# Kernel tuning notes

Hardware: AMD Instinct MI355X
Metric: run time of the kernel (lower is better)

Reference implementation:

```python
import jax, jax.numpy as jnp
import numpy as np

B, T, C = 4, 2048, 1024
H = 16
DH = C // H  # 64


def setup_inputs() -> dict:
    key = jax.random.key(0)
    ks = jax.random.split(key, 10)
    s_in = 1.0 / np.sqrt(C)
    x = jax.random.normal(ks[0], (B, T, C), dtype=jnp.float32)
    # stacked per-head projection weights: [H, C, DH]
    Wq = jax.random.normal(ks[1], (H, C, DH), dtype=jnp.float32) * s_in
    bq = jnp.zeros((H, DH), dtype=jnp.float32)
    Wk = jax.random.normal(ks[2], (H, C, DH), dtype=jnp.float32) * s_in
    bk = jnp.zeros((H, DH), dtype=jnp.float32)
    Wv = jax.random.normal(ks[3], (H, C, DH), dtype=jnp.float32) * s_in
    bv = jnp.zeros((H, DH), dtype=jnp.float32)
    Wo = jax.random.normal(ks[4], (C, C), dtype=jnp.float32) * s_in
    bo = jnp.zeros((C,), dtype=jnp.float32)
    return {"x": x, "Wq": Wq, "bq": bq, "Wk": Wk, "bk": bk,
            "Wv": Wv, "bv": bv, "Wo": Wo, "bo": bo}


def reference(x, Wq, bq, Wk, bk, Wv, bv, Wo, bo):
    # per-head projections: (B,T,C) x (H,C,DH) -> (B,H,T,DH)
    q = jnp.einsum('btc,hcd->bhtd', x, Wq) + bq[None, :, None, :]
    k = jnp.einsum('btc,hcd->bhtd', x, Wk) + bk[None, :, None, :]
    v = jnp.einsum('btc,hcd->bhtd', x, Wv) + bv[None, :, None, :]
    # scores scaled by C**-0.5 (C = full input embedding dim, as in source)
    scale = jnp.float32(C) ** -0.5
    scores = jnp.einsum('bhtd,bhsd->bhts', q, k) * scale  # (B,H,T,T)
    causal = jnp.tril(jnp.ones((T, T), dtype=bool))
    scores = jnp.where(causal, scores, -jnp.inf)
    attn = jax.nn.softmax(scores, axis=-1)
    out = jnp.einsum('bhts,bhsd->bhtd', attn, v)  # (B,H,T,DH)
    out = out.transpose(0, 2, 1, 3).reshape(B, T, C)  # concat heads
    return out @ Wo + bo
```

## Files before the change

### kernel.cpp

```cpp
#include <hip/hip_runtime.h>
#include <hip/hip_bf16.h>

#define TDIM 2048
#define BDIM 4
#define CDIM 1024
#define HDIM 16
#define DH   64

typedef __hip_bfloat16 bf16;
typedef __attribute__((ext_vector_type(8))) short bf16x8;
typedef __attribute__((ext_vector_type(4))) short bf16x4;
typedef __attribute__((ext_vector_type(4))) float f32x4;

__device__ __forceinline__ void async_ld16(const bf16* g, bf16* l) {
    __builtin_amdgcn_global_load_lds(
        (const __attribute__((address_space(1))) unsigned int*)g,
        (__attribute__((address_space(3))) unsigned int*)l, 16, 0, 0);
}

__device__ __forceinline__ unsigned short bf16bits(float x) {
    bf16 b = __float2bfloat16(x);
    return *(unsigned short*)&b;
}

__device__ __forceinline__ f32x4 mfma_16x16x16_bf16(bf16x4 a, bf16x4 b, f32x4 c) {
#if __has_builtin(__builtin_amdgcn_mfma_f32_16x16x16_bf16)
    return __builtin_amdgcn_mfma_f32_16x16x16_bf16(a, b, c, 0, 0, 0);
#elif __has_builtin(__builtin_amdgcn_mfma_f32_16x16x16bf16_1k)
    return __builtin_amdgcn_mfma_f32_16x16x16bf16_1k(a, b, c, 0, 0, 0);
#else
    asm volatile("v_mfma_f32_16x16x16_bf16 %0, %1, %2, %0"
                 : "+v"(c) : "v"(a), "v"(b));
    return c;
#endif
}

__global__ void convert_x4(const float4* __restrict__ src, ushort4* __restrict__ dst, int n4) {
    int i = blockIdx.x * blockDim.x + threadIdx.x;
    if (i >= n4) return;
    float4 v = src[i];
    ushort4 o;
    o.x = bf16bits(v.x); o.y = bf16bits(v.y);
    o.z = bf16bits(v.z); o.w = bf16bits(v.w);
    dst[i] = o;
}

__global__ void convert_biases(const float* __restrict__ b0, const float* __restrict__ b1,
                               const float* __restrict__ b2, const float* __restrict__ b3,
                               bf16* __restrict__ dst) {
    int i = blockIdx.x * blockDim.x + threadIdx.x;
    int which = i >> 10, j = i & 1023;
    const float* src = (which == 0) ? b0 : (which == 1) ? b1 : (which == 2) ? b2 : b3;
    dst[i] = __float2bfloat16(src[j]);
}

__global__ __launch_bounds__(256) void transpose_qkv_kernel(
    const float* __restrict__ Wq, const float* __restrict__ Wk, const float* __restrict__ Wv,
    bf16* __restrict__ WqT, bf16* __restrict__ WkT, bf16* __restrict__ WvT) {
    __shared__ float tile[64][65];
    const int which = blockIdx.z >> 4, h = blockIdx.z & 15;
    const float* W  = ((which == 0) ? Wq  : (which == 1) ? Wk  : Wv)  + (size_t)h * CDIM * DH;
    bf16*        WT = ((which == 0) ? WqT : (which == 1) ? WkT : WvT) + (size_t)h * CDIM * DH;
    const int c0 = blockIdx.x * 64;
    for (int it = 0; it < 16; it++) {
        int e = it * 256 + threadIdx.x;
        int r = e >> 6, col = e & 63;
        tile[r][col] = W[(size_t)(c0 + r) * DH + col];
    }
    __syncthreads();
    for (int it = 0; it < 16; it++) {
        int e = it * 256 + threadIdx.x;
        int r = e >> 6, col = e & 63;
        WT[(size_t)r * CDIM + c0 + col] = __float2bfloat16(tile[col][r]);
    }
}

__global__ __launch_bounds__(256) void transpose_wo_kernel(
    const float* __restrict__ W, bf16* __restrict__ WT) {
    __shared__ float tile[64][65];
    const int c0 = blockIdx.x * 64, d0 = blockIdx.y * 64;
    for (int it = 0; it < 16; it++) {
        int e = it * 256 + threadIdx.x;
        int r = e >> 6, col = e & 63;
        tile[r][col] = W[(size_t)(c0 + r) * CDIM + d0 + col];
    }
    __syncthreads();
    for (int it = 0; it < 16; it++) {
        int e = it * 256 + threadIdx.x;
        int r = e >> 6, col = e & 63;
        WT[(size_t)(d0 + r) * CDIM + c0 + col] = __float2bfloat16(tile[col][r]);
    }
}

__global__ __launch_bounds__(256) void transpose_v_kernel(
    const bf16* __restrict__ V, bf16* __restrict__ Vt) {
    __shared__ unsigned short tile[64][65];
    const int bh = blockIdx.y, t0 = blockIdx.x * 64;
    const unsigned short* Vp  = (const unsigned short*)V + ((size_t)bh * TDIM + t0) * DH;
    unsigned short*       Vtp = (unsigned short*)Vt + (size_t)bh * DH * TDIM;
    for (int it = 0; it < 16; it++) {
        int e = it * 256 + threadIdx.x;
        int r = e >> 6, c = e & 63;
        tile[r][c] = Vp[(size_t)r * DH + c];
    }
    __syncthreads();
    for (int it = 0; it < 16; it++) {
        int e = it * 256 + threadIdx.x;
        int r = e >> 6, c = e & 63;
        Vtp[(size_t)r * TDIM + t0 + c] = tile[c][r];
    }
}

__global__ __launch_bounds__(256) void proj_qkv_kernel(
    const bf16* __restrict__ X,
    const bf16* __restrict__ WqT, const bf16* __restrict__ WkT, const bf16* __restrict__ WvT,
    const bf16* __restrict__ bq,  const bf16* __restrict__ bk,  const bf16* __restrict__ bvv,
    bf16* __restrict__ Qo, bf16* __restrict__ Ko, bf16* __restrict__ Vo)
{
    const int z = blockIdx.z;
    const bf16* Bt   = (z == 0) ? WqT : (z == 1) ? WkT : WvT;
    const bf16* bias = (z == 0) ? bq  : (z == 1) ? bk  : bvv;

    __shared__ __align__(16) bf16 As[128 * 32];
    __shared__ __align__(16) bf16 Bs[128 * 32];

    const int tid  = threadIdx.x;
    const int lane = tid & 63;
    const int wave = tid >> 6;
    const int wr = wave >> 1, wc = wave & 1;
    const int l15 = lane & 15, quad = lane >> 4;

    const int blockM = blockIdx.y * 128;
    const int blockN = blockIdx.x * 128;

    f32x4 acc[4][4];
    for (int i = 0; i < 4; i++)
        for (int j = 0; j < 4; j++)
            acc[i][j] = (f32x4){0.f, 0.f, 0.f, 0.f};

    const int srow = lane >> 2, scol = (lane & 3) * 8;
    for (int k0 = 0; k0 < CDIM; k0 += 32) {
        for (int cc = 0; cc < 2; cc++) {
            int chunk = wave * 2 + cc;
            int row = chunk * 16 + srow;
            async_ld16(&X [(size_t)(blockM + row) * CDIM + k0 + scol], &As[chunk * 512]);
            async_ld16(&Bt[(size_t)(blockN + row) * CDIM + k0 + scol], &Bs[chunk * 512]);
        }
        __syncthreads();

        bf16x8 af[4], bfr[4];
        for (int mi = 0; mi < 4; mi++)
            af[mi] = *(const bf16x8*)&As[(wr * 64 + mi * 16 + l15) * 32 + quad * 8];
        for (int ni = 0; ni < 4; ni++)
            bfr[ni] = *(const bf16x8*)&Bs[(wc * 64 + ni * 16 + l15) * 32 + quad * 8];

        for (int mi = 0; mi < 4; mi++)
            for (int ni = 0; ni < 4; ni++)
                acc[mi][ni] = __builtin_amdgcn_mfma_f32_16x16x32_bf16(
                    af[mi], bfr[ni], acc[mi][ni], 0, 0, 0);
        __syncthreads();
    }

    for (int mi = 0; mi < 4; mi++) {
        int mbase = blockM + wr * 64 + mi * 16 + quad * 4;
        for (int ni = 0; ni < 4; ni++) {
            int n = blockN + wc * 64 + ni * 16 + l15;
            float bval = __bfloat162float(bias[n]);
            int h = n >> 6, d = n & 63;
            for (int r = 0; r < 4; r++) {
                int mm = mbase + r;
                int b = mm >> 11, t = mm & 2047;
                float val = acc[mi][ni][r] + bval;
                size_t idx = (((size_t)b * HDIM + h) * TDIM + t) * DH + d;
                if (z == 0)      Qo[idx] = __float2bfloat16(val * 0.03125f);
                else if (z == 1) Ko[idx] = __float2bfloat16(val);
                else             Vo[idx] = __float2bfloat16(val);
            }
        }
    }
}

__global__ __launch_bounds__(256) void proj_out_kernel(
    const bf16* __restrict__ X, const bf16* __restrict__ Bt,
    const bf16* __restrict__ bias, float* __restrict__ Out)
{
    __shared__ __align__(16) bf16 As[128 * 32];
    __shared__ __align__(16) bf16 Bs[128 * 32];

    const int tid  = threadIdx.x;
    const int lane = tid & 63;
    const int wave = tid >> 6;
    const int wr = wave >> 1, wc = wave & 1;
    const int l15 = lane & 15, quad = lane >> 4;

    const int blockM = blockIdx.y * 128;
    const int blockN = blockIdx.x * 128;

    f32x4 acc[4][4];
    for (int i = 0; i < 4; i++)
        for (int j = 0; j < 4; j++)
            acc[i][j] = (f32x4){0.f, 0.f, 0.f, 0.f};

    const int srow = lane >> 2, scol = (lane & 3) * 8;
    for (int k0 = 0; k0 < CDIM; k0 += 32) {
        for (int cc = 0; cc < 2; cc++) {
            int chunk = wave * 2 + cc;
            int row = chunk * 16 + srow;
            async_ld16(&X [(size_t)(blockM + row) * CDIM + k0 + scol], &As[chunk * 512]);
            async_ld16(&Bt[(size_t)(blockN + row) * CDIM + k0 + scol], &Bs[chunk * 512]);
        }
        __syncthreads();

        bf16x8 af[4], bfr[4];
        for (int mi = 0; mi < 4; mi++)
            af[mi] = *(const bf16x8*)&As[(wr * 64 + mi * 16 + l15) * 32 + quad * 8];
        for (int ni = 0; ni < 4; ni++)
            bfr[ni] = *(const bf16x8*)&Bs[(wc * 64 + ni * 16 + l15) * 32 + quad * 8];

        for (int mi = 0; mi < 4; mi++)
            for (int ni = 0; ni < 4; ni++)
                acc[mi][ni] = __builtin_amdgcn_mfma_f32_16x16x32_bf16(
                    af[mi], bfr[ni], acc[mi][ni], 0, 0, 0);
        __syncthreads();
    }

    for (int mi = 0; mi < 4; mi++) {
        int mbase = blockM + wr * 64 + mi * 16 + quad * 4;
        for (int ni = 0; ni < 4; ni++) {
            int n = blockN + wc * 64 + ni * 16 + l15;
            float bval = __bfloat162float(bias[n]);
            for (int r = 0; r < 4; r++)
                Out[(size_t)(mbase + r) * CDIM + n] = acc[mi][ni][r] + bval;
        }
    }
}

__global__ __launch_bounds__(256, 4) void attn_kernel(
    const bf16* __restrict__ Q, const bf16* __restrict__ Kb,
    const bf16* __restrict__ Vt, bf16* __restrict__ Y)
{
    const int bh    = blockIdx.y;
    const int qT    = (int)gridDim.x - 1 - blockIdx.x;
    const int qBase = qT * 64;
    const int tid  = threadIdx.x;
    const int lane = tid & 63, wave = tid >> 6;
    const int l15 = lane & 15, quad = lane >> 4;

    __shared__ __align__(16) bf16 Ks[64 * 72];
    __shared__ __align__(16) bf16 Vs[64 * 72];

    const size_t qrow = (size_t)bh * TDIM + qBase + wave * 16 + l15;
    const bf16x8 qf0 = *(const bf16x8*)&Q[qrow * DH + quad * 8];
    const bf16x8 qf1 = *(const bf16x8*)&Q[qrow * DH + 32 + quad * 8];

    f32x4 o[4];
    for (int mt = 0; mt < 4; mt++) o[mt] = (f32x4){0.f, 0.f, 0.f, 0.f};
    float lsum = 0.f;

    const int r0 = tid >> 3, kc0 = (tid & 7) * 8;

    const int nkt  = qT + 1;
    const int qloc = wave * 16 + l15;

    uint4 kreg0 = *(const uint4*)&Kb[((size_t)bh * TDIM + r0) * DH + kc0];
    uint4 kreg1 = *(const uint4*)&Kb[((size_t)bh * TDIM + r0 + 32) * DH + kc0];
    uint4 vreg0 = *(const uint4*)&Vt[((size_t)bh * DH + r0) * TDIM + kc0];
    uint4 vreg1 = *(const uint4*)&Vt[((size_t)bh * DH + r0 + 32) * TDIM + kc0];

    for (int kt = 0; kt < nkt; kt++) {
        *(uint4*)&Ks[r0 * 72 + kc0]        = kreg0;
        *(uint4*)&Ks[(r0 + 32) * 72 + kc0] = kreg1;
        *(uint4*)&Vs[r0 * 72 + kc0]        = vreg0;
        *(uint4*)&Vs[(r0 + 32) * 72 + kc0] = vreg1;
        __syncthreads();

        if (kt + 1 < nkt) {
            const int nb = (kt + 1) * 64;
            kreg0 = *(const uint4*)&Kb[((size_t)bh * TDIM + nb + r0) * DH + kc0];
            kreg1 = *(const uint4*)&Kb[((size_t)bh * TDIM + nb + r0 + 32) * DH + kc0];
            vreg0 = *(const uint4*)&Vt[((size_t)bh * DH + r0) * TDIM + nb + kc0];
            vreg1 = *(const uint4*)&Vt[((size_t)bh * DH + r0 + 32) * TDIM + nb + kc0];
        }

        const bool diag = (kt == qT);
        for (int nt = 0; nt < 4; nt++) {
            bf16x8 kf0 = *(const bf16x8*)&Ks[(nt * 16 + l15) * 72 + quad * 8];
            bf16x8 kf1 = *(const bf16x8*)&Ks[(nt * 16 + l15) * 72 + 32 + quad * 8];
            bf16x4 vA[4];
            for (int mt = 0; mt < 4; mt++)
                vA[mt] = *(const bf16x4*)&Vs[(mt * 16 + l15) * 72 + nt * 16 + quad * 4];

            f32x4 s = (f32x4){0.f, 0.f, 0.f, 0.f};
            s = __builtin_amdgcn_mfma_f32_16x16x32_bf16(kf0, qf0, s, 0, 0, 0);
            s = __builtin_amdgcn_mfma_f32_16x16x32_bf16(kf1, qf1, s, 0, 0, 0);

            bf16x4 pb;
            for (int r = 0; r < 4; r++) {
                float pe = __expf(s[r]);
                if (diag && (nt * 16 + quad * 4 + r > qloc)) pe = 0.f;
                lsum += pe;
                pb[r] = (short)bf16bits(pe);
            }
            for (int mt = 0; mt < 4; mt++)
                o[mt] = mfma_16x16x16_bf16(vA[mt], pb, o[mt]);
        }
        __syncthreads();
    }

    float v = lsum;
    v += __shfl_xor(v, 16, 64);
    v += __shfl_xor(v, 32, 64);
    const float inv = 1.0f / v;

    unsigned short* sm = (unsigned short*)Ks;
    for (int mt = 0; mt < 4; mt++) {
        unsigned short pk[4];
        for (int r = 0; r < 4; r++) pk[r] = bf16bits(o[mt][r] * inv);
        *(ushort4*)&sm[(wave * 16 + l15) * 72 + mt * 16 + quad * 4] = *(ushort4*)pk;
    }
    const int b = bh >> 4, h = bh & 15;
    const int qq = lane >> 2, part = lane & 3;
    const int t = qBase + wave * 16 + qq;
    uint4 c0 = *(const uint4*)&sm[(wave * 16 + qq) * 72 + part * 16];
    uint4 c1 = *(const uint4*)&sm[(wave * 16 + qq) * 72 + part * 16 + 8];
    *(uint4*)&Y[((size_t)b * TDIM + t) * CDIM + h * DH + part * 16]     = c0;
    *(uint4*)&Y[((size_t)b * TDIM + t) * CDIM + h * DH + part * 16 + 8] = c1;
}

extern "C" void kernel_launch(void* const* d_in, const int* in_sizes, int n_in,
                              void* d_out, int out_size, void* d_ws, size_t ws_size,
                              hipStream_t stream) {
    (void)in_sizes; (void)n_in; (void)out_size; (void)ws_size;

    char* ws = (char*)d_ws;
    const size_t SZ_BHTD = (size_t)BDIM * HDIM * TDIM * DH * sizeof(bf16);
    const size_t SZ_W    = (size_t)HDIM * CDIM * DH * sizeof(bf16);
    bf16* Qb  = (bf16*)(ws);
    bf16* Kb  = (bf16*)(ws + SZ_BHTD);
    bf16* Vt  = (bf16*)(ws + 2 * SZ_BHTD);
    bf16* Y   = (bf16*)(ws + 3 * SZ_BHTD);
    bf16* WqT = (bf16*)(ws + 4 * SZ_BHTD);
    bf16* WkT = (bf16*)(ws + 4 * SZ_BHTD + SZ_W);
    bf16* WvT = (bf16*)(ws + 4 * SZ_BHTD + 2 * SZ_W);
    bf16* WoT = (bf16*)(ws + 4 * SZ_BHTD + 3 * SZ_W);
    bf16* xC  = (bf16*)(ws + 4 * SZ_BHTD + 4 * SZ_W);
    bf16* bqC = (bf16*)(ws + 5 * SZ_BHTD + 4 * SZ_W);
    bf16* bkC = bqC + 1024;
    bf16* bvC = bqC + 2048;
    bf16* boC = bqC + 3072;
    bf16* Vb  = (bf16*)d_out;

    const int nX4 = (BDIM * TDIM * CDIM) / 4;
    convert_x4<<<nX4 / 256, 256, 0, stream>>>((const float4*)d_in[0], (ushort4*)xC, nX4);
    convert_biases<<<16, 256, 0, stream>>>((const float*)d_in[2], (const float*)d_in[4],
                                           (const float*)d_in[6], (const float*)d_in[8], bqC);

    transpose_qkv_kernel<<<dim3(CDIM / 64, 1, 48), 256, 0, stream>>>(
        (const float*)d_in[1], (const float*)d_in[3], (const float*)d_in[5], WqT, WkT, WvT);
    transpose_wo_kernel<<<dim3(CDIM / 64, CDIM / 64), 256, 0, stream>>>(
        (const float*)d_in[7], WoT);

    dim3 gq(CDIM / 128, (BDIM * TDIM) / 128, 3);
    proj_qkv_kernel<<<gq, 256, 0, stream>>>(xC, WqT, WkT, WvT, bqC, bkC, bvC, Qb, Kb, Vb);

    transpose_v_kernel<<<dim3(TDIM / 64, BDIM * HDIM), 256, 0, stream>>>(Vb, Vt);

    attn_kernel<<<dim3(TDIM / 64, BDIM * HDIM), 256, 0, stream>>>(Qb, Kb, Vt, Y);

    proj_out_kernel<<<dim3(CDIM / 128, (BDIM * TDIM) / 128), 256, 0, stream>>>(
        Y, WoT, boC, (float*)d_out);
}
```

Before: 327.8 us.

## Load K/V tiles via async global-to-LDS with XOR-swizzled layout

Replaces the register-staged K/V prefetch (global load into VGPRs, then store to padded LDS) in the attention kernel with direct global_load_lds transfers into an unpadded 64-wide LDS tile that uses an XOR swizzle to avoid bank conflicts. The read-side indices for K and V fragments are adjusted to match the swizzle. This frees registers and drops the LDS write instructions. However, it also removes the previous double-buffered prefetch, so the load for each tile is now issued just before the barrier with no overlap. The epilogue's 72-stride staging through smem may also alias the 64-stride buffer layout.

```diff
diff --git a/kernel.cpp b/kernel.cpp
--- a/kernel.cpp
+++ b/kernel.cpp
@@ -246,8 +246,9 @@
     const int lane = tid & 63, wave = tid >> 6;
     const int l15 = lane & 15, quad = lane >> 4;
 
-    __shared__ __align__(16) bf16 Ks[64 * 72];
-    __shared__ __align__(16) bf16 Vs[64 * 72];
+    __shared__ __align__(16) bf16 smem[2 * 64 * 64];
+    bf16* Ks = smem;
+    bf16* Vs = smem + 64 * 64;
 
     const size_t qrow = (size_t)bh * TDIM + qBase + wave * 16 + l15;
     const bf16x8 qf0 = *(const bf16x8*)&Q[qrow * DH + quad * 8];
@@ -257,38 +258,40 @@
     for (int mt = 0; mt < 4; mt++) o[mt] = (f32x4){0.f, 0.f, 0.f, 0.f};
     float lsum = 0.f;
 
-    const int r0 = tid >> 3, kc0 = (tid & 7) * 8;
+    const int srow = (wave << 4) + (lane >> 3);
+    const int ssc  = (((lane & 7) ^ (lane >> 3)) << 3);
+    const bf16* kSrc0 = Kb + ((size_t)bh * TDIM + srow) * DH + ssc;
+    const bf16* vSrc0 = Vt + ((size_t)bh * DH + srow) * TDIM + ssc;
+
+    const int swA   = l15 & 7;
+    const int kcol0 = ((quad ^ swA) << 3);
+    const int kcol1 = (((4 + quad) ^ swA) << 3);
+    const int u2    = quad >> 1, intra = ((quad & 1) << 2);
 
     const int nkt  = qT + 1;
     const int qloc = wave * 16 + l15;
 
-    uint4 kreg0 = *(const uint4*)&Kb[((size_t)bh * TDIM + r0) * DH + kc0];
-    uint4 kreg1 = *(const uint4*)&Kb[((size_t)bh * TDIM + r0 + 32) * DH + kc0];
-    uint4 vreg0 = *(const uint4*)&Vt[((size_t)bh * DH + r0) * TDIM + kc0];
-    uint4 vreg1 = *(const uint4*)&Vt[((size_t)bh * DH + r0 + 32) * TDIM + kc0];
-
     for (int kt = 0; kt < nkt; kt++) {
-        *(uint4*)&Ks[r0 * 72 + kc0]        = kreg0;
-        *(uint4*)&Ks[(r0 + 32) * 72 + kc0] = kreg1;
-        *(uint4*)&Vs[r0 * 72 + kc0]        = vreg0;
-        *(uint4*)&Vs[(r0 + 32) * 72 + kc0] = vreg1;
-        __syncthreads();
-
-        if (kt + 1 < nkt) {
-            const int nb = (kt + 1) * 64;
-            kreg0 = *(const uint4*)&Kb[((size_t)bh * TDIM + nb + r0) * DH + kc0];
-            kreg1 = *(const uint4*)&Kb[((size_t)bh * TDIM + nb + r0 + 32) * DH + kc0];
-            vreg0 = *(const uint4*)&Vt[((size_t)bh * DH + r0) * TDIM + nb + kc0];
-            vreg1 = *(const uint4*)&Vt[((size_t)bh * DH + r0 + 32) * TDIM + nb + kc0];
-        }
+        {
+            const bf16* kS = kSrc0 + (size_t)kt * 64 * DH;
+            const bf16* vS = vSrc0 + (size_t)kt * 64;
+            bf16* kD = Ks + (wave * 16) * 64;
+            bf16* vD = Vs + (wave * 16) * 64;
+            async_ld16(kS,            kD);
+            async_ld16(kS + 8 * DH,   kD + 8 * 64);
+            async_ld16(vS,            vD);
+            async_ld16(vS + 8 * TDIM, vD + 8 * 64);
+        }
+        __syncthreads();
 
         const bool diag = (kt == qT);
         for (int nt = 0; nt < 4; nt++) {
-            bf16x8 kf0 = *(const bf16x8*)&Ks[(nt * 16 + l15) * 72 + quad * 8];
-            bf16x8 kf1 = *(const bf16x8*)&Ks[(nt * 16 + l15) * 72 + 32 + quad * 8];
+            bf16x8 kf0 = *(const bf16x8*)&Ks[(nt * 16 + l15) * 64 + kcol0];
+            bf16x8 kf1 = *(const bf16x8*)&Ks[(nt * 16 + l15) * 64 + kcol1];
             bf16x4 vA[4];
             for (int mt = 0; mt < 4; mt++)
-                vA[mt] = *(const bf16x4*)&Vs[(mt * 16 + l15) * 72 + nt * 16 + quad * 4];
+                vA[mt] = *(const bf16x4*)&Vs[(mt * 16 + l15) * 64 +
+                                             (((nt * 2 + u2) ^ swA) << 3) + intra];
 
             f32x4 s = (f32x4){0.f, 0.f, 0.f, 0.f};
             s = __builtin_amdgcn_mfma_f32_16x16x32_bf16(kf0, qf0, s, 0, 0, 0);
@@ -312,7 +315,7 @@
     v += __shfl_xor(v, 32, 64);
     const float inv = 1.0f / v;
 
-    unsigned short* sm = (unsigned short*)Ks;
+    unsigned short* sm = (unsigned short*)smem;
     for (int mt = 0; mt < 4; mt++) {
         unsigned short pk[4];
         for (int r = 0; r < 4; r++) pk[r] = bf16bits(o[mt][r] * inv);
```

Measured after the change: 306.4 us. -6.5%, faster.
